# Performance work log

Measured on AMD Instinct MI355X. Metric: run time of the kernel, lower is better.

The kernel has to match this reference:

```python
import jax, jax.numpy as jnp
import numpy as np

C_FEAT = 64


def _dilation_indices(seq_len, dilation):
    # Static (trace-time) replication of _generate_dilation_mask, as index set.
    side = int(round(seq_len ** (1.0 / 3.0)))  # 32 for N=32768
    g = np.arange(side)
    zz, yy, xx = np.meshgrid(g, g, g, indexing='ij')
    coords = np.stack([zz, yy, xx], axis=-1).astype(np.float32)
    center = side // 2
    d = np.sqrt(((coords - center) ** 2).sum(-1))
    mask = ((d % dilation) == 0) | (d == 0)
    return jnp.asarray(np.nonzero(mask.reshape(-1))[0], dtype=jnp.int32)


def _dst_block(x, qkv_w, qkv_b, proj_w, proj_b, idx):
    # x: [B, N, C]; attention restricted to the dilation-sampled token subset.
    B, N, C = x.shape
    qkv = x @ qkv_w.T + qkv_b                      # [B, N, 3C]
    q, k, v = jnp.split(qkv, 3, axis=-1)           # each [B, N, C]
    qs, ks, vs = q[:, idx], k[:, idx], v[:, idx]   # [B, M, C] (gather == dense-then-mask)
    scale = 1.0 / jnp.sqrt(jnp.asarray(C, x.dtype))
    attn = jax.nn.softmax(jnp.einsum('bmc,bnc->bmn', qs, ks) * scale, axis=-1)
    y = jnp.einsum('bmn,bnc->bmc', attn, vs)       # [B, M, C]
    out = (y @ proj_w.T + proj_b) + y              # proj + residual
    # scatter sampled tokens back so the token grid stays N (see notes)
    return x.at[:, idx].set(out)


def _lerp_axis(x, axis, out_size):
    # 1-D linear interp along `axis`, align_corners=True
    n = x.shape[axis]
    pos = jnp.arange(out_size, dtype=jnp.float32) * ((n - 1) / (out_size - 1))
    i0 = jnp.floor(pos).astype(jnp.int32)
    i1 = jnp.minimum(i0 + 1, n - 1)
    w = pos - i0.astype(jnp.float32)
    shp = [1] * x.ndim
    shp[axis] = out_size
    w = w.reshape(shp)
    return jnp.take(x, i0, axis=axis) * (1.0 - w) + jnp.take(x, i1, axis=axis) * w


def _forward(x, w_patch, b_patch, pos_embed,
             qkv_w1, qkv_b1, proj_w1, proj_b1,
             qkv_w2, qkv_b2, proj_w2, proj_b2,
             qkv_w3, qkv_b3, proj_w3, proj_b3):
    h = jax.lax.conv_general_dilated(
        x, w_patch, window_strides=(4, 4, 4), padding='VALID',
        dimension_numbers=('NCDHW', 'OIDHW', 'NCDHW'))
    h = h + b_patch[None, :, None, None, None]          # [B, C, 32, 32, 32]
    B, C, Z, Y, X = h.shape
    N = Z * Y * X
    t = h.reshape(B, C, N).transpose(0, 2, 1)
    t = t + pos_embed.reshape(1, C, N).transpose(0, 2, 1)
    for (qw, qb, pw, pb, dil) in ((qkv_w1, qkv_b1, proj_w1, proj_b1, 2),
                                  (qkv_w2, qkv_b2, proj_w2, proj_b2, 4),
                                  (qkv_w3, qkv_b3, proj_w3, proj_b3, 6)):
        idx = _dilation_indices(N, dil)
        t = _dst_block(t, qw, qb, pw, pb, idx)
    h = t.transpose(0, 2, 1).reshape(B, C, Z, Y, X)
    # trilinear upsample x4, align_corners=True
    for ax in (2, 3, 4):
        h = _lerp_axis(h, ax, h.shape[ax] * 4)
    return h


def setup_inputs() -> dict:
    key = jax.random.key(0)
    ks = jax.random.split(key, 12)
    C = C_FEAT
    d = {
        'x': jax.random.normal(ks[0], (1, 1, 128, 128, 128), jnp.float32),
        'w_patch': jax.random.normal(ks[1], (C, 1, 4, 4, 4), jnp.float32) * 0.1,
        'b_patch': jnp.zeros((C,), jnp.float32),
        'pos_embed': jax.random.normal(ks[2], (1, C, 32, 32, 32), jnp.float32) * 0.02,
    }
    for i in range(3):
        d[f'qkv_w{i+1}'] = jax.random.normal(ks[3 + 3 * i], (3 * C, C), jnp.float32) * 0.05
        d[f'qkv_b{i+1}'] = jnp.zeros((3 * C,), jnp.float32)
        d[f'proj_w{i+1}'] = jax.random.normal(ks[4 + 3 * i], (C, C), jnp.float32) * 0.05
        d[f'proj_b{i+1}'] = jnp.zeros((C,), jnp.float32)
    return d


def reference(x, w_patch, b_patch, pos_embed,
              qkv_w1, qkv_b1, proj_w1, proj_b1,
              qkv_w2, qkv_b2, proj_w2, proj_b2,
              qkv_w3, qkv_b3, proj_w3, proj_b3):
    return _forward(x, w_patch, b_patch, pos_embed,
                    qkv_w1, qkv_b1, proj_w1, proj_b1,
                    qkv_w2, qkv_b2, proj_w2, proj_b2,
                    qkv_w3, qkv_b3, proj_w3, proj_b3)
```

## Files before the change

kernel.cpp:

```cpp
#include <hip/hip_runtime.h>
#include <cmath>

#define NTOK 32768
#define CF   64
#define TSP  66

__global__ void prep_kernel(const float* __restrict__ qw0, const float* __restrict__ qb0,
                            const float* __restrict__ pw0, const float* __restrict__ pb0,
                            const float* __restrict__ qw1, const float* __restrict__ qb1,
                            const float* __restrict__ pw1, const float* __restrict__ pb1,
                            const float* __restrict__ qw2, const float* __restrict__ qb2,
                            const float* __restrict__ pw2, const float* __restrict__ pb2,
                            float* __restrict__ consts) {
    int di = blockIdx.x;
    const float* qw = di == 0 ? qw0 : (di == 1 ? qw1 : qw2);
    const float* qb = di == 0 ? qb0 : (di == 1 ? qb1 : qb2);
    const float* pw = di == 0 ? pw0 : (di == 1 ? pw1 : pw2);
    const float* pb = di == 0 ? pb0 : (di == 1 ? pb1 : pb2);
    float* base = consts + di * 8448;
    float* At  = base;
    float* Bt  = base + 4096;
    float* bqp = base + 8192;
    float* w2  = base + 8256;
    float* bb  = base + 8320;
    float* c0  = base + 8384;
    int tid = threadIdx.x;
    const float scale = 0.125f;
    for (int o = tid; o < 4096; o += 256) {
        int k = o >> 6, c = o & 63;
        float a = 0.f;
        for (int m = 0; m < 64; ++m)
            a += qw[(64 + m) * 64 + c] * qw[m * 64 + k];
        At[k * 64 + c] = scale * a;
    }
    for (int o = tid; o < 4096; o += 256) {
        int c = o >> 6, k = o & 63;
        float b = 0.f;
        for (int m = 0; m < 64; ++m) {
            float pp = pw[c * 64 + m] + (c == m ? 1.f : 0.f);
            b += pp * qw[(128 + m) * 64 + k];
        }
        Bt[k * 64 + c] = b;
    }
    if (tid < 64) {
        int c = tid;
        float a = 0.f, w = 0.f, b = 0.f;
        for (int m = 0; m < 64; ++m) {
            a += qw[(64 + m) * 64 + c] * qb[m];
            w += qb[64 + m] * qw[m * 64 + c];
            float pp = pw[c * 64 + m] + (c == m ? 1.f : 0.f);
            b += pp * qb[128 + m];
        }
        bqp[c] = scale * a;
        w2[c]  = scale * w;
        bb[c]  = b + pb[c];
        if (c == 0) {
            float s = 0.f;
            for (int m = 0; m < 64; ++m) s += qb[m] * qb[64 + m];
            c0[0] = scale * s;
        }
    }
}

__global__ __launch_bounds__(256) void patch_kernel(const float* __restrict__ x,
                             const float* __restrict__ w,
                             const float* __restrict__ bias,
                             const float* __restrict__ pos,
                             float* __restrict__ tnc,
                             float* __restrict__ tcn) {
    __shared__ float xsT[64 * 32];
    __shared__ float wT[64 * 65];
    __shared__ float res[64 * 33];
    int tid = threadIdx.x;
    int z = blockIdx.x >> 5, y = blockIdx.x & 31;

    for (int k = tid; k < 4096; k += 256) {
        int c = k >> 6, tap = k & 63;
        wT[tap * 65 + c] = w[k];
    }
    #pragma unroll
    for (int p = 0; p < 2; ++p) {
        int q = tid + p * 256;
        int r = q >> 5;
        int col4 = q & 31;
        int dz = r >> 2, dy = r & 3;
        const float4* src = (const float4*)(x + (size_t)((z * 4 + dz) * 128 + (y * 4 + dy)) * 128);
        float4 v = src[col4];
        int tb = dz * 16 + dy * 4;
        xsT[(tb + 0) * 32 + col4] = v.x;
        xsT[(tb + 1) * 32 + col4] = v.y;
        xsT[(tb + 2) * 32 + col4] = v.z;
        xsT[(tb + 3) * 32 + col4] = v.w;
    }
    __syncthreads();

    int xx = tid & 31;
    int ch = tid >> 5;
    int nb = z * 1024 + y * 32;
    #pragma unroll
    for (int p = 0; p < 8; ++p) {
        int c = ch + p * 8;
        float acc = bias[c];
        #pragma unroll
        for (int k = 0; k < 64; ++k)
            acc += xsT[k * 32 + xx] * wT[k * 65 + c];
        res[c * 33 + xx] = acc + pos[c * NTOK + nb + xx];
    }
    __syncthreads();
    for (int q = tid; q < 2048; q += 256) {
        int tok = q >> 6, c = q & 63;
        tnc[(size_t)(nb + tok) * 64 + c] = res[c * 33 + tok];
    }
    for (int q = tid; q < 2048; q += 256) {
        int c = q >> 5, x2 = q & 31;
        tcn[(size_t)c * NTOK + nb + x2] = res[c * 33 + x2];
    }
}

__global__ __launch_bounds__(256) void dst_kernel(const float* __restrict__ tnc,
                           const float* __restrict__ cbase,
                           const int* __restrict__ idx,
                           float* __restrict__ yout, int M) {
    __shared__ float ts[280 * TSP];
    __shared__ float kqs[4 * 64];
    const float* At  = cbase;
    const float* Bt  = cbase + 4096;
    const float* bqp = cbase + 8192;
    const float* w2v = cbase + 8256;
    const float* bbv = cbase + 8320;
    const float* c0v = cbase + 8384;
    int tid = threadIdx.x;
    for (int q = tid; q < M * 16; q += 256) {
        int j = q >> 4, c4 = (q & 15) << 2;
        const float4 v = *(const float4*)(tnc + (size_t)idx[j] * 64 + c4);
        float* d = ts + j * TSP + c4;
        d[0] = v.x; d[1] = v.y; d[2] = v.z; d[3] = v.w;
    }
    __syncthreads();
    int w = tid >> 6, lane = tid & 63;
    int qi = blockIdx.x * 4 + w;
    if (qi >= M) return;
    const float* trow = ts + qi * TSP;
    float kq = bqp[lane];
    #pragma unroll 16
    for (int k = 0; k < 64; ++k)
        kq += At[k * 64 + lane] * trow[k];
    kqs[w * 64 + lane] = kq;
    float sb = w2v[lane] * trow[lane];
    #pragma unroll
    for (int off = 32; off > 0; off >>= 1) sb += __shfl_xor(sb, off);
    sb += c0v[0];

    float p[5];
    float mx = -INFINITY;
    const float2* kq2 = (const float2*)(kqs + w * 64);
    #pragma unroll
    for (int it = 0; it < 5; ++it) {
        int j = it * 64 + lane;
        p[it] = -INFINITY;
        if (j < M) {
            const float2* tr2 = (const float2*)(ts + j * TSP);
            float s = sb;
            #pragma unroll 8
            for (int c = 0; c < 32; ++c) {
                float2 a = kq2[c]; float2 b = tr2[c];
                s += a.x * b.x + a.y * b.y;
            }
            p[it] = s; mx = fmaxf(mx, s);
        }
    }
    #pragma unroll
    for (int off = 32; off > 0; off >>= 1) mx = fmaxf(mx, __shfl_xor(mx, off));
    float ssum = 0.f;
    #pragma unroll
    for (int it = 0; it < 5; ++it) {
        int j = it * 64 + lane;
        float e = (j < M) ? expf(p[it] - mx) : 0.f;
        p[it] = e; ssum += e;
    }
    #pragma unroll
    for (int off = 32; off > 0; off >>= 1) ssum += __shfl_xor(ssum, off);
    float inv = 1.f / ssum;

    float u = 0.f;
    #pragma unroll
    for (int it = 0; it < 5; ++it) {
        int jb = it * 64;
        if (jb < M) {
            int cnt = min(64, M - jb);
            for (int jj = 0; jj < cnt; ++jj) {
                float pj = __shfl(p[it], jj);
                u += pj * ts[(jb + jj) * TSP + lane];
            }
        }
    }
    u *= inv;
    kqs[w * 64 + lane] = u;
    float o = bbv[lane];
    const float2* u2 = (const float2*)(kqs + w * 64);
    #pragma unroll 8
    for (int k = 0; k < 32; ++k) {
        float2 uu = u2[k];
        o += Bt[(2 * k) * 64 + lane] * uu.x + Bt[(2 * k + 1) * 64 + lane] * uu.y;
    }
    yout[qi * 64 + lane] = o;
}

__global__ void scatter_kernel(const float* __restrict__ yout,
                               float* __restrict__ tnc,
                               float* __restrict__ tcn,
                               const int* __restrict__ idx) {
    int i = blockIdx.x, c = threadIdx.x;
    int n = idx[i];
    float v = yout[i * 64 + c];
    tnc[(size_t)n * 64 + c] = v;
    tcn[(size_t)c * NTOK + n] = v;
}

__global__ void upsample_kernel(const float* __restrict__ h, float* __restrict__ out) {
    int bc = blockIdx.x;
    int c = bc >> 7, zo = bc & 127;
    __shared__ float pz[1024];
    __shared__ float wtab[128];
    __shared__ int   itab[128];
    int tid = threadIdx.x;
    const float scale = (float)(31.0 / 127.0);
    if (tid < 128) {
        float p = (float)tid * scale;
        int i0 = (int)floorf(p);
        if (i0 > 31) i0 = 31;
        itab[tid] = i0;
        wtab[tid] = p - (float)i0;
    }
    float pzf = (float)zo * scale;
    int zi0 = (int)floorf(pzf);
    if (zi0 > 31) zi0 = 31;
    int zi1 = min(zi0 + 1, 31);
    float wz = pzf - (float)zi0;
    const float4* pl0 = (const float4*)(h + (c * 32 + zi0) * 1024);
    const float4* pl1 = (const float4*)(h + (c * 32 + zi1) * 1024);
    float4 a = pl0[tid];
    float4 b = pl1[tid];
    float4 r;
    r.x = a.x * (1.f - wz) + b.x * wz;
    r.y = a.y * (1.f - wz) + b.y * wz;
    r.z = a.z * (1.f - wz) + b.z * wz;
    r.w = a.w * (1.f - wz) + b.w * wz;
    ((float4*)pz)[tid] = r;
    __syncthreads();
    float4* o = (float4*)(out + (size_t)(c * 128 + zo) * 16384);
    for (int q = 0; q < 16; ++q) {
        int Q = q * 256 + tid;
        int yo = Q >> 5, xq = Q & 31;
        int yi0 = itab[yo];
        float wy = wtab[yo];
        int yi1 = min(yi0 + 1, 31);
        const float* r0 = pz + yi0 * 32;
        const float* r1 = pz + yi1 * 32;
        float vv[4];
        #pragma unroll
        for (int k = 0; k < 4; ++k) {
            int xo = xq * 4 + k;
            int xi0 = itab[xo];
            float wx = wtab[xo];
            int xi1 = min(xi0 + 1, 31);
            float v0 = r0[xi0] * (1.f - wx) + r0[xi1] * wx;
            float v1 = r1[xi0] * (1.f - wx) + r1[xi1] * wx;
            vv[k] = v0 * (1.f - wy) + v1 * wy;
        }
        float4 v; v.x = vv[0]; v.y = vv[1]; v.z = vv[2]; v.w = vv[3];
        o[Q] = v;
    }
}

extern "C" void kernel_launch(void* const* d_in, const int* in_sizes, int n_in,
                              void* d_out, int out_size, void* d_ws, size_t ws_size,
                              hipStream_t stream) {
    const float* x       = (const float*)d_in[0];
    const float* w_patch = (const float*)d_in[1];
    const float* b_patch = (const float*)d_in[2];
    const float* pos     = (const float*)d_in[3];
    float* out = (float*)d_out;

    char* ws = (char*)d_ws;
    if (ws_size < (size_t)(20u << 20)) return;
    float* tcn    = (float*)ws;
    float* tnc    = (float*)(ws + (8u << 20));
    float* yout   = (float*)(ws + (16u << 20));
    int*   idx    = (int*)  (ws + (17u << 20));
    float* consts = (float*)(ws + (18u << 20));

    static int h_idx[3 * 1024];
    int M[3];
    for (int di = 0; di < 3; ++di) {
        int dil = 2 * (di + 1), cnt = 0;
        for (int n = 0; n < NTOK; ++n) {
            int z = n >> 10, yy = (n >> 5) & 31, xx = n & 31;
            int a = z - 16, b = yy - 16, c = xx - 16;
            int dd = a * a + b * b + c * c;
            int s = (int)(std::sqrt((double)dd) + 0.5);
            if (s * s == dd && (s % dil) == 0) h_idx[di * 1024 + cnt++] = n;
        }
        M[di] = cnt;
    }
    hipMemcpyAsync(idx, h_idx, sizeof(h_idx), hipMemcpyHostToDevice, stream);

    prep_kernel<<<3, 256, 0, stream>>>(
        (const float*)d_in[4],  (const float*)d_in[5],  (const float*)d_in[6],  (const float*)d_in[7],
        (const float*)d_in[8],  (const float*)d_in[9],  (const float*)d_in[10], (const float*)d_in[11],
        (const float*)d_in[12], (const float*)d_in[13], (const float*)d_in[14], (const float*)d_in[15],
        consts);
    patch_kernel<<<1024, 256, 0, stream>>>(x, w_patch, b_patch, pos, tnc, tcn);
    for (int di = 0; di < 3; ++di) {
        dst_kernel<<<(M[di] + 3) / 4, 256, 0, stream>>>(tnc, consts + di * 8448, idx + di * 1024, yout, M[di]);
        scatter_kernel<<<M[di], 64, 0, stream>>>(yout, tnc, tcn, idx + di * 1024);
    }
    upsample_kernel<<<CF * 128, 256, 0, stream>>>(tcn, out);
}
```

Before: 721.6 us.

## Fuse prep into patch kernel, chain DST stages without scatter, precompute upsample x-lerp

The weight-folding prep work now runs as extra blocks of the patch embedding kernel, which removes one launch and spreads the work across many threads. The separate scatter kernels are gone. Each DST stage gathers its inputs from the previous stage's compact output buffer through host-computed index maps, and writes to the channel-major grid only tokens that later stages will not overwrite. The upsample kernel first interpolates along x into shared memory, then does vectorized y-lerps with nontemporal stores. The cost is extra host-side index bookkeeping and more shared memory in the upsample kernel.

Result: faster. 650.4 us (-9.9%).

```diff
diff --git a/kernel.cpp b/kernel.cpp
--- a/kernel.cpp
+++ b/kernel.cpp
@@ -5,75 +5,79 @@
 #define CF   64
 #define TSP  66
 
-__global__ void prep_kernel(const float* __restrict__ qw0, const float* __restrict__ qb0,
-                            const float* __restrict__ pw0, const float* __restrict__ pb0,
-                            const float* __restrict__ qw1, const float* __restrict__ qb1,
-                            const float* __restrict__ pw1, const float* __restrict__ pb1,
-                            const float* __restrict__ qw2, const float* __restrict__ qb2,
-                            const float* __restrict__ pw2, const float* __restrict__ pb2,
-                            float* __restrict__ consts) {
-    int di = blockIdx.x;
-    const float* qw = di == 0 ? qw0 : (di == 1 ? qw1 : qw2);
-    const float* qb = di == 0 ? qb0 : (di == 1 ? qb1 : qb2);
-    const float* pw = di == 0 ? pw0 : (di == 1 ? pw1 : pw2);
-    const float* pb = di == 0 ? pb0 : (di == 1 ? pb1 : pb2);
-    float* base = consts + di * 8448;
-    float* At  = base;
-    float* Bt  = base + 4096;
-    float* bqp = base + 8192;
-    float* w2  = base + 8256;
-    float* bb  = base + 8320;
-    float* c0  = base + 8384;
-    int tid = threadIdx.x;
-    const float scale = 0.125f;
-    for (int o = tid; o < 4096; o += 256) {
-        int k = o >> 6, c = o & 63;
-        float a = 0.f;
-        for (int m = 0; m < 64; ++m)
-            a += qw[(64 + m) * 64 + c] * qw[m * 64 + k];
-        At[k * 64 + c] = scale * a;
-    }
-    for (int o = tid; o < 4096; o += 256) {
-        int c = o >> 6, k = o & 63;
-        float b = 0.f;
-        for (int m = 0; m < 64; ++m) {
-            float pp = pw[c * 64 + m] + (c == m ? 1.f : 0.f);
-            b += pp * qw[(128 + m) * 64 + k];
-        }
-        Bt[k * 64 + c] = b;
-    }
-    if (tid < 64) {
-        int c = tid;
-        float a = 0.f, w = 0.f, b = 0.f;
-        for (int m = 0; m < 64; ++m) {
-            a += qw[(64 + m) * 64 + c] * qb[m];
-            w += qb[64 + m] * qw[m * 64 + c];
-            float pp = pw[c * 64 + m] + (c == m ? 1.f : 0.f);
-            b += pp * qb[128 + m];
-        }
-        bqp[c] = scale * a;
-        w2[c]  = scale * w;
-        bb[c]  = b + pb[c];
-        if (c == 0) {
-            float s = 0.f;
-            for (int m = 0; m < 64; ++m) s += qb[m] * qb[64 + m];
-            c0[0] = scale * s;
-        }
-    }
-}
-
-__global__ __launch_bounds__(256) void patch_kernel(const float* __restrict__ x,
-                             const float* __restrict__ w,
-                             const float* __restrict__ bias,
-                             const float* __restrict__ pos,
-                             float* __restrict__ tnc,
-                             float* __restrict__ tcn) {
+typedef __attribute__((ext_vector_type(4))) float f32x4;
+
+#define OFF_IDX2 0
+#define OFF_T4   512
+#define OFF_T6   768
+#define OFF_G1   1024
+#define OFF_G2   1280
+#define OFF_W0   1536
+#define OFF_W1   2048
+#define BLOB_INTS 2112
+
+__global__ __launch_bounds__(256) void patch_prep_kernel(
+    const float* __restrict__ x, const float* __restrict__ w,
+    const float* __restrict__ bias, const float* __restrict__ pos,
+    float* __restrict__ tnc, float* __restrict__ tcn,
+    const float* __restrict__ qw0, const float* __restrict__ qb0,
+    const float* __restrict__ pw0, const float* __restrict__ pb0,
+    const float* __restrict__ qw1, const float* __restrict__ qb1,
+    const float* __restrict__ pw1, const float* __restrict__ pb1,
+    const float* __restrict__ qw2, const float* __restrict__ qb2,
+    const float* __restrict__ pw2, const float* __restrict__ pb2,
+    float* __restrict__ consts) {
     __shared__ float xsT[64 * 32];
     __shared__ float wT[64 * 65];
     __shared__ float res[64 * 33];
     int tid = threadIdx.x;
+
+    if (blockIdx.x >= 1024) {
+        int gid = (blockIdx.x - 1024) * 256 + tid;
+        if (gid >= 3 * 8257) return;
+        int di = gid / 8257, o = gid % 8257;
+        const float* qw = di == 0 ? qw0 : (di == 1 ? qw1 : qw2);
+        const float* qb = di == 0 ? qb0 : (di == 1 ? qb1 : qb2);
+        const float* pw = di == 0 ? pw0 : (di == 1 ? pw1 : pw2);
+        const float* pb = di == 0 ? pb0 : (di == 1 ? pb1 : pb2);
+        float* base = consts + di * 8448;
+        const float scale = 0.125f;
+        if (o < 4096) {
+            int k = o >> 6, c = o & 63;
+            float a = 0.f;
+            for (int m = 0; m < 64; ++m)
+                a += qw[(64 + m) * 64 + c] * qw[m * 64 + k];
+            base[o] = scale * a;
+        } else if (o < 8192) {
+            int oo = o - 4096;
+            int c = oo >> 6, k = oo & 63;
+            float b = 0.f;
+            for (int m = 0; m < 64; ++m) {
+                float pp = pw[c * 64 + m] + (c == m ? 1.f : 0.f);
+                b += pp * qw[(128 + m) * 64 + k];
+            }
+            base[4096 + k * 64 + c] = b;
+        } else if (o < 8256) {
+            int c = o - 8192;
+            float a = 0.f, wv = 0.f, b = 0.f;
+            for (int m = 0; m < 64; ++m) {
+                a += qw[(64 + m) * 64 + c] * qb[m];
+                wv += qb[64 + m] * qw[m * 64 + c];
+                float pp = pw[c * 64 + m] + (c == m ? 1.f : 0.f);
+                b += pp * qb[128 + m];
+            }
+            base[8192 + c] = scale * a;
+            base[8256 + c] = scale * wv;
+            base[8320 + c] = b + pb[c];
+        } else {
+            float s = 0.f;
+            for (int m = 0; m < 64; ++m) s += qb[m] * qb[64 + m];
+            base[8384] = scale * s;
+        }
+        return;
+    }
+
     int z = blockIdx.x >> 5, y = blockIdx.x & 31;
-
     for (int k = tid; k < 4096; k += 256) {
         int c = k >> 6, tap = k & 63;
         wT[tap * 65 + c] = w[k];
@@ -117,10 +121,11 @@
     }
 }
 
-__global__ __launch_bounds__(256) void dst_kernel(const float* __restrict__ tnc,
-                           const float* __restrict__ cbase,
-                           const int* __restrict__ idx,
-                           float* __restrict__ yout, int M) {
+__global__ __launch_bounds__(256) void dst_kernel(
+    const float* __restrict__ gp, const int* __restrict__ gidx,
+    const float* __restrict__ cbase, float* __restrict__ ydst,
+    const int* __restrict__ tok, const int* __restrict__ wflag,
+    float* __restrict__ tcn, int M) {
     __shared__ float ts[280 * TSP];
     __shared__ float kqs[4 * 64];
     const float* At  = cbase;
@@ -132,7 +137,7 @@
     int tid = threadIdx.x;
     for (int q = tid; q < M * 16; q += 256) {
         int j = q >> 4, c4 = (q & 15) << 2;
-        const float4 v = *(const float4*)(tnc + (size_t)idx[j] * 64 + c4);
+        const float4 v = *(const float4*)(gp + (size_t)gidx[j] * 64 + c4);
         float* d = ts + j * TSP + c4;
         d[0] = v.x; d[1] = v.y; d[2] = v.z; d[3] = v.w;
     }
@@ -203,24 +208,16 @@
         float2 uu = u2[k];
         o += Bt[(2 * k) * 64 + lane] * uu.x + Bt[(2 * k + 1) * 64 + lane] * uu.y;
     }
-    yout[qi * 64 + lane] = o;
+    if (ydst) ydst[qi * 64 + lane] = o;
+    if (!wflag || wflag[qi]) tcn[(size_t)lane * NTOK + tok[qi]] = o;
 }
 
-__global__ void scatter_kernel(const float* __restrict__ yout,
-                               float* __restrict__ tnc,
-                               float* __restrict__ tcn,
-                               const int* __restrict__ idx) {
-    int i = blockIdx.x, c = threadIdx.x;
-    int n = idx[i];
-    float v = yout[i * 64 + c];
-    tnc[(size_t)n * 64 + c] = v;
-    tcn[(size_t)c * NTOK + n] = v;
-}
-
-__global__ void upsample_kernel(const float* __restrict__ h, float* __restrict__ out) {
+__global__ __launch_bounds__(256) void upsample_kernel(const float* __restrict__ h,
+                                                       float* __restrict__ out) {
     int bc = blockIdx.x;
     int c = bc >> 7, zo = bc & 127;
     __shared__ float pz[1024];
+    __shared__ float pzx[32 * 128];
     __shared__ float wtab[128];
     __shared__ int   itab[128];
     int tid = threadIdx.x;
@@ -237,39 +234,32 @@
     if (zi0 > 31) zi0 = 31;
     int zi1 = min(zi0 + 1, 31);
     float wz = pzf - (float)zi0;
-    const float4* pl0 = (const float4*)(h + (c * 32 + zi0) * 1024);
-    const float4* pl1 = (const float4*)(h + (c * 32 + zi1) * 1024);
-    float4 a = pl0[tid];
-    float4 b = pl1[tid];
-    float4 r;
-    r.x = a.x * (1.f - wz) + b.x * wz;
-    r.y = a.y * (1.f - wz) + b.y * wz;
-    r.z = a.z * (1.f - wz) + b.z * wz;
-    r.w = a.w * (1.f - wz) + b.w * wz;
-    ((float4*)pz)[tid] = r;
-    __syncthreads();
-    float4* o = (float4*)(out + (size_t)(c * 128 + zo) * 16384);
+    const f32x4* pl0 = (const f32x4*)(h + (size_t)(c * 32 + zi0) * 1024);
+    const f32x4* pl1 = (const f32x4*)(h + (size_t)(c * 32 + zi1) * 1024);
+    f32x4 a = pl0[tid];
+    f32x4 b = pl1[tid];
+    ((f32x4*)pz)[tid] = a * (1.f - wz) + b * wz;
+    __syncthreads();
+    for (int q = tid; q < 4096; q += 256) {
+        int yi = q >> 7, xo = q & 127;
+        int xi0 = itab[xo];
+        int xi1 = min(xi0 + 1, 31);
+        float wx = wtab[xo];
+        const float* r = pz + yi * 32;
+        pzx[yi * 128 + xo] = r[xi0] * (1.f - wx) + r[xi1] * wx;
+    }
+    __syncthreads();
+    f32x4* o = (f32x4*)(out + (size_t)(c * 128 + zo) * 16384);
     for (int q = 0; q < 16; ++q) {
         int Q = q * 256 + tid;
         int yo = Q >> 5, xq = Q & 31;
         int yi0 = itab[yo];
         float wy = wtab[yo];
         int yi1 = min(yi0 + 1, 31);
-        const float* r0 = pz + yi0 * 32;
-        const float* r1 = pz + yi1 * 32;
-        float vv[4];
-        #pragma unroll
-        for (int k = 0; k < 4; ++k) {
-            int xo = xq * 4 + k;
-            int xi0 = itab[xo];
-            float wx = wtab[xo];
-            int xi1 = min(xi0 + 1, 31);
-            float v0 = r0[xi0] * (1.f - wx) + r0[xi1] * wx;
-            float v1 = r1[xi0] * (1.f - wx) + r1[xi1] * wx;
-            vv[k] = v0 * (1.f - wy) + v1 * wy;
-        }
-        float4 v; v.x = vv[0]; v.y = vv[1]; v.z = vv[2]; v.w = vv[3];
-        o[Q] = v;
+        f32x4 v0 = *(const f32x4*)(pzx + yi0 * 128 + xq * 4);
+        f32x4 v1 = *(const f32x4*)(pzx + yi1 * 128 + xq * 4);
+        f32x4 v = v0 * (1.f - wy) + v1 * wy;
+        __builtin_nontemporal_store(v, o + Q);
     }
 }
 
@@ -286,34 +276,59 @@
     if (ws_size < (size_t)(20u << 20)) return;
     float* tcn    = (float*)ws;
     float* tnc    = (float*)(ws + (8u << 20));
-    float* yout   = (float*)(ws + (16u << 20));
-    int*   idx    = (int*)  (ws + (17u << 20));
+    float* yb     = (float*)(ws + (16u << 20));
+    int*   blob   = (int*)  (ws + (17u << 20));
     float* consts = (float*)(ws + (18u << 20));
 
-    static int h_idx[3 * 1024];
-    int M[3];
-    for (int di = 0; di < 3; ++di) {
-        int dil = 2 * (di + 1), cnt = 0;
-        for (int n = 0; n < NTOK; ++n) {
-            int z = n >> 10, yy = (n >> 5) & 31, xx = n & 31;
-            int a = z - 16, b = yy - 16, c = xx - 16;
-            int dd = a * a + b * b + c * c;
-            int s = (int)(std::sqrt((double)dd) + 0.5);
-            if (s * s == dd && (s % dil) == 0) h_idx[di * 1024 + cnt++] = n;
-        }
-        M[di] = cnt;
-    }
-    hipMemcpyAsync(idx, h_idx, sizeof(h_idx), hipMemcpyHostToDevice, stream);
-
-    prep_kernel<<<3, 256, 0, stream>>>(
+    static int h_blob[BLOB_INTS];
+    static int pos2[NTOK], pos4[NTOK];
+    static unsigned char f4[NTOK], f6[NTOK];
+    int c2 = 0, c4 = 0, c6 = 0;
+    for (int n = 0; n < NTOK; ++n) {
+        int z = n >> 10, yy = (n >> 5) & 31, xx = n & 31;
+        int a = z - 16, b = yy - 16, c = xx - 16;
+        int dd = a * a + b * b + c * c;
+        int s = (int)(std::sqrt((double)dd) + 0.5);
+        bool ps = (s * s == dd);
+        bool s2 = ps && (s % 2 == 0);
+        bool s4 = ps && (s % 4 == 0);
+        bool s6 = ps && (s % 6 == 0);
+        f4[n] = s4; f6[n] = s6;
+        if (s2) { pos2[n] = c2; h_blob[OFF_IDX2 + c2] = n; c2++; }
+        if (s4) { pos4[n] = c4; h_blob[OFF_T4 + c4] = n; c4++; }
+        if (s6) { h_blob[OFF_T6 + c6] = n; c6++; }
+    }
+    for (int j = 0; j < c4; ++j) {
+        int n = h_blob[OFF_T4 + j];
+        h_blob[OFF_G1 + j] = pos2[n];
+        h_blob[OFF_W1 + j] = f6[n] ? 0 : 1;
+    }
+    for (int j = 0; j < c6; ++j) {
+        int n = h_blob[OFF_T6 + j];
+        h_blob[OFF_G2 + j] = f4[n] ? (c2 + pos4[n]) : pos2[n];
+    }
+    for (int q = 0; q < c2; ++q) {
+        int n = h_blob[OFF_IDX2 + q];
+        h_blob[OFF_W0 + q] = (f4[n] || f6[n]) ? 0 : 1;
+    }
+    hipMemcpyAsync(blob, h_blob, sizeof(h_blob), hipMemcpyHostToDevice, stream);
+
+    patch_prep_kernel<<<1024 + 97, 256, 0, stream>>>(
+        x, w_patch, b_patch, pos, tnc, tcn,
         (const float*)d_in[4],  (const float*)d_in[5],  (const float*)d_in[6],  (const float*)d_in[7],
         (const float*)d_in[8],  (const float*)d_in[9],  (const float*)d_in[10], (const float*)d_in[11],
         (const float*)d_in[12], (const float*)d_in[13], (const float*)d_in[14], (const float*)d_in[15],
         consts);
-    patch_kernel<<<1024, 256, 0, stream>>>(x, w_patch, b_patch, pos, tnc, tcn);
-    for (int di = 0; di < 3; ++di) {
-        dst_kernel<<<(M[di] + 3) / 4, 256, 0, stream>>>(tnc, consts + di * 8448, idx + di * 1024, yout, M[di]);
-        scatter_kernel<<<M[di], 64, 0, stream>>>(yout, tnc, tcn, idx + di * 1024);
-    }
+
+    dst_kernel<<<(c2 + 3) / 4, 256, 0, stream>>>(
+        tnc, blob + OFF_IDX2, consts + 0 * 8448, yb,
+        blob + OFF_IDX2, blob + OFF_W0, tcn, c2);
+    dst_kernel<<<(c4 + 3) / 4, 256, 0, stream>>>(
+        yb, blob + OFF_G1, consts + 1 * 8448, yb + (size_t)c2 * 64,
+        blob + OFF_T4, blob + OFF_W1, tcn, c4);
+    dst_kernel<<<(c6 + 3) / 4, 256, 0, stream>>>(
+        yb, blob + OFF_G2, consts + 2 * 8448, nullptr,
+        blob + OFF_T6, nullptr, tcn, c6);
+
     upsample_kernel<<<CF * 128, 256, 0, stream>>>(tcn, out);
 }
```
